# Optimization experiments

Measured on AMD Instinct MI355X. Metric: run time of the kernel, lower is better.

The kernel has to match this reference:

```python
import jax, jax.numpy as jnp
import numpy as np

V, C, D = 25, 64, 64          # joints, in_channels, out_channels
N, T = 64, 300                # batch, frames
WEIGHT = 2
GROUPS = [[0, 12], [13, 24]]
BN_EPS = 1e-5


def _inner_shift(A, graph_group, node, channels, weight):
    """Faithful numpy port of Modified_grouped_shift_gcn.inner_shift."""
    index_array = np.arange(node * channels).reshape(node, channels)
    copy = index_array.copy()
    for grp in graph_group:
        lb, ub = int(np.min(grp)), int(np.max(grp)) + 1
        for i in range(lb, ub):
            cur = A[i].copy()
            cur[i] = 0
            neighbors = np.nonzero(cur)[0]
            j = 0
            ci = i - lb + 1
            while j < channels:
                nxt = ci % (ub - lb) + lb
                if j < weight:
                    j += weight
                elif nxt == i:
                    j += weight
                    ci += 1
                elif nxt in neighbors:
                    index_array[i][j:j + weight] = copy[nxt][j:j + weight]
                    j += weight
                    ci += 1
                else:
                    index_array[i][j] = copy[nxt][j]
                    j += 1
                    ci += 1
    return index_array.flatten()


def _adjacency():
    # chain skeleton with self loops, binarized as in __init__
    A = np.zeros((V, V), dtype=np.float64)
    for i in range(V - 1):
        A[i, i + 1] = 1.0
        A[i + 1, i] = 1.0
    np.fill_diagonal(A, 1.0)
    return A


def setup_inputs() -> dict:
    key = jax.random.key(0)
    k0, k1, k2, k3 = jax.random.split(key, 4)
    A = _adjacency()
    shift_in = jnp.asarray(_inner_shift(A, GROUPS, V, C, WEIGHT), dtype=jnp.int32)
    shift_out = jnp.asarray(_inner_shift(A, GROUPS, V, D, WEIGHT), dtype=jnp.int32)
    x0 = jax.random.normal(k0, (N, C, T, V), dtype=jnp.float32)
    feature_mask = 0.1 * jax.random.normal(k1, (1, V, C), dtype=jnp.float32)
    W = jax.random.normal(k2, (C, D), dtype=jnp.float32) * np.float32(np.sqrt(1.0 / D))
    b = 0.01 * jax.random.normal(k3, (1, 1, D), dtype=jnp.float32)
    gamma = jnp.ones((V * D,), dtype=jnp.float32)
    beta = jnp.zeros((V * D,), dtype=jnp.float32)
    return {"x0": x0, "feature_mask": feature_mask, "W": W, "b": b,
            "gamma": gamma, "beta": beta,
            "shift_in": shift_in, "shift_out": shift_out}


def reference(x0, feature_mask, W, b, gamma, beta, shift_in, shift_out):
    n, c, t, v = x0.shape
    # (n, c, t, v) -> (n*t, v*c)
    x = jnp.transpose(x0, (0, 2, 3, 1)).reshape(n * t, v * c)
    # channel-wise shift gather (precomputed permutation)
    x = x[:, shift_in].reshape(n * t, v, c)
    # learned feature mask
    x = x * (jnp.tanh(feature_mask) + 1.0)
    # pointwise linear + bias
    x = jnp.einsum('nvc,cd->nvd', x, W) + b
    x = x.reshape(n * t, v * W.shape[1])
    # second shift gather
    x = x[:, shift_out]
    # BatchNorm1d, training mode (biased batch stats)
    mean = jnp.mean(x, axis=0)
    var = jnp.var(x, axis=0)
    x = (x - mean) * jax.lax.rsqrt(var + BN_EPS) * gamma + beta
    # back to (n, d, t, v), residual (in==out so down is identity), relu
    x = x.reshape(n, t, v, W.shape[1]).transpose(0, 3, 1, 2)
    return jax.nn.relu(x + x0)
```

## Files before the change

kernel.cpp:

```cpp
#include <hip/hip_runtime.h>
#include <math.h>

#define V_ 25
#define C_ 64
#define D_ 64
#define N_ 64
#define T_ 300
#define R_ (N_*T_)
#define K_ (V_*C_)
#define BN_EPS 1e-5f

#define WS_GM     0
#define WS_SCALE  1600
#define WS_SHIFT  3200
#define WS_VP     4800
#define WS_SUM    6400
#define WS_SQ     8000
#define WS_WBF    9600

#define P1_BLOCKS 1200

using bf16x8 = __attribute__((ext_vector_type(8))) short;
using f32x4  = __attribute__((ext_vector_type(4))) float;

__device__ __forceinline__ unsigned short f2bf(float f) {
    unsigned u = __float_as_uint(f);
    return (unsigned short)((u + 0x7FFFu + ((u >> 16) & 1u)) >> 16);
}

__global__ __launch_bounds__(256) void prep_tables(
    const float* __restrict__ fm, const float* __restrict__ W,
    const int* __restrict__ s_in, float* __restrict__ ws)
{
    int idx = blockIdx.x * 256 + threadIdx.x;
    if (idx < K_) {
        int jj  = s_in[idx];
        int off = (jj & 63) * 100 + (jj >> 6);
        unsigned mk = (unsigned)f2bf(tanhf(fm[idx]) + 1.0f);
        ((unsigned*)ws)[WS_GM + idx] = (mk << 16) | (unsigned)off;
    }
    if (idx < C_ * D_) ((unsigned short*)(ws + WS_WBF))[idx] = f2bf(W[idx]);
}

__global__ __launch_bounds__(256) void stats_reduce(
    const float* __restrict__ pbuf, float* __restrict__ ws)
{
    __shared__ float red[256];
    int jq = threadIdx.x & 15;
    int bq = threadIdx.x >> 4;
    int j  = blockIdx.x * 16 + jq;
    const float* p = pbuf + (size_t)(bq * 75) * 3200 + j;
    float s = 0.f;
    #pragma unroll 5
    for (int k = 0; k < 75; ++k)
        s += p[(size_t)k * 3200];
    red[threadIdx.x] = s;
    __syncthreads();
    if (bq < 8) red[threadIdx.x] += red[threadIdx.x + 128];
    __syncthreads();
    if (bq < 4) red[threadIdx.x] += red[threadIdx.x + 64];
    __syncthreads();
    if (bq < 2) red[threadIdx.x] += red[threadIdx.x + 32];
    __syncthreads();
    if (bq == 0) ws[WS_SUM + j] = red[jq] + red[jq + 16];
}

__global__ __launch_bounds__(256) void prep_scale_kernel(
    const float* __restrict__ gamma, const float* __restrict__ beta,
    const int* __restrict__ s_out, float* __restrict__ ws)
{
    int kk = blockIdx.x * 256 + threadIdx.x;
    if (kk < K_) {
        int dd = kk / 25;
        int v  = kk - dd * 25;
        int k  = v * 64 + dd;
        int jj = s_out[k];
        float mean = ws[WS_SUM + jj] * (1.0f / (float)R_);
        float var  = fmaf(-mean, mean, ws[WS_SQ + jj] * (1.0f / (float)R_));
        float inv  = rsqrtf(var + BN_EPS);
        float sc   = gamma[k] * inv;
        ws[WS_SCALE + kk] = sc;
        ws[WS_SHIFT + kk] = beta[k] - mean * sc;
        ((int*)ws)[WS_VP + kk] = jj;
    }
}

__device__ __forceinline__ void stage_xs(
    const float* __restrict__ xwin, float4* xs4, int tid)
{
    const float4* s4 = (const float4*)xwin;
    #pragma unroll
    for (int i = 0; i < 7; ++i) {
        int idx = i * 256 + tid;
        if (idx < 1600) {
            int c = idx / 25;
            int r = idx - c * 25;
            xs4[c * 25 + r] = s4[c * 1875 + r];
        }
    }
}

__device__ __forceinline__ void load_gmr(
    const unsigned* __restrict__ gmt, unsigned gmr[28], int lane, int w)
{
    int jw = lane & 3;
    int vh = lane >> 4;
    #pragma unroll
    for (int i = 0; i < 14; ++i) {
        int combo = i * 4 + w;
        int T  = combo >> 2;
        int q2 = combo & 3;
        int t  = T >> 1;
        int c0 = (T & 1) * 32 + q2 * 8 + jw * 2;
        int v  = t * 4 + vh;
        int kb = (v < V_) ? (v * 64 + c0) : c0;
        gmr[2 * i]     = gmt[kb];
        gmr[2 * i + 1] = gmt[kb + 1];
    }
}

__device__ __forceinline__ void build_afm(
    const float* xs, unsigned* a_fm32, const unsigned gmr[28], int lane, int w)
{
    int m  = lane >> 2;
    int jw = lane & 3;
    int dt = m & 3;
    #pragma unroll
    for (int i = 0; i < 14; ++i) {
        int combo = i * 4 + w;
        int T  = combo >> 2;
        int q2 = combo & 3;
        unsigned g0 = gmr[2 * i], g1 = gmr[2 * i + 1];
        float m0 = __uint_as_float(g0 & 0xFFFF0000u);
        float m1 = __uint_as_float(g1 & 0xFFFF0000u);
        float f0 = xs[(g0 & 0xFFFFu) + dt * 25] * m0;
        float f1 = xs[(g1 & 0xFFFFu) + dt * 25] * m1;
        a_fm32[(T * 64 + q2 * 16 + m) * 4 + jw] =
            (unsigned)f2bf(f0) | ((unsigned)f2bf(f1) << 16);
    }
}

__global__ __launch_bounds__(256, 4) void pass1_stats(
    const float* __restrict__ x0, const float* __restrict__ bg,
    const float* __restrict__ ws, float* __restrict__ pbuf)
{
    __shared__ __align__(16) float4 xs4[1600];
    __shared__ __align__(16) unsigned a_fm32[3584];
    const float* xs = (const float*)xs4;
    const bf16x8* afp = (const bf16x8*)a_fm32;

    int tid = threadIdx.x;
    int lane = tid & 63, w = tid >> 6;
    int l15 = lane & 15, q = lane >> 4;
    int d = w * 16 + l15;

    const unsigned short* Wbf = (const unsigned short*)(ws + WS_WBF);
    bf16x8 bfrag0, bfrag1;
    #pragma unroll
    for (int j = 0; j < 8; ++j) {
        bfrag0[j] = (short)Wbf[(q * 8 + j) * 64 + d];
        bfrag1[j] = (short)Wbf[(32 + q * 8 + j) * 64 + d];
    }
    float breg = bg[d];

    unsigned gmr[28];
    load_gmr((const unsigned*)ws + WS_GM, gmr, lane, w);

    float sums[7], sqs[7];
    #pragma unroll
    for (int t = 0; t < 7; ++t) { sums[t] = 0.f; sqs[t] = 0.f; }

    #pragma unroll 1
    for (int st = 0; st < 4; ++st) {
        int r0 = blockIdx.x * 16 + st * 4;
        int n  = r0 / 300;
        int t0 = r0 - n * 300;
        const float* xwin = x0 + (size_t)n * 480000 + t0 * 25;

        stage_xs(xwin, xs4, tid);
        __syncthreads();
        build_afm(xs, a_fm32, gmr, lane, w);
        __syncthreads();

        #pragma unroll
        for (int t = 0; t < 7; ++t) {
            bf16x8 a0 = afp[(t * 2 + 0) * 64 + lane];
            bf16x8 a1 = afp[(t * 2 + 1) * 64 + lane];
            f32x4 acc = {0.f, 0.f, 0.f, 0.f};
            acc = __builtin_amdgcn_mfma_f32_16x16x32_bf16(a0, bfrag0, acc, 0, 0, 0);
            acc = __builtin_amdgcn_mfma_f32_16x16x32_bf16(a1, bfrag1, acc, 0, 0, 0);
            #pragma unroll
            for (int r = 0; r < 4; ++r) {
                float y = acc[r] + breg;
                sums[t] += y;
                sqs[t]   = fmaf(y, y, sqs[t]);
            }
        }
        __syncthreads();
    }

    float* pout = pbuf + (size_t)blockIdx.x * 3200;
    #pragma unroll
    for (int t = 0; t < 7; ++t) {
        int v = t * 4 + q;
        if (v < V_) {
            __builtin_nontemporal_store(sums[t], &pout[v * 64 + d]);
            __builtin_nontemporal_store(sqs[t],  &pout[1600 + v * 64 + d]);
        }
    }
}

__global__ __launch_bounds__(256, 4) void pass2_out(
    const float* __restrict__ x0, const float* __restrict__ bg,
    const float* __restrict__ ws, float* __restrict__ out)
{
    __shared__ __align__(16) char smem[25600 + 14336];
    float4* xs4   = (float4*)smem;
    const float* xs = (const float*)smem;
    float* y_lds  = (float*)smem;
    unsigned* a_fm32 = (unsigned*)(smem + 25600);
    const bf16x8* afp = (const bf16x8*)a_fm32;

    int tid = threadIdx.x;
    int lane = tid & 63, w = tid >> 6;
    int l15 = lane & 15, q = lane >> 4;
    int d = w * 16 + l15;

    const unsigned short* Wbf = (const unsigned short*)(ws + WS_WBF);
    bf16x8 bfrag0, bfrag1;
    #pragma unroll
    for (int j = 0; j < 8; ++j) {
        bfrag0[j] = (short)Wbf[(q * 8 + j) * 64 + d];
        bfrag1[j] = (short)Wbf[(32 + q * 8 + j) * 64 + d];
    }
    float breg = bg[d];

    unsigned gmr[28];
    load_gmr((const unsigned*)ws + WS_GM, gmr, lane, w);

    int r0 = blockIdx.x * 4;
    int n  = r0 / 300;
    int t0 = r0 - n * 300;
    const float* xwin = x0 + (size_t)n * 480000 + t0 * 25;

    stage_xs(xwin, xs4, tid);
    __syncthreads();
    build_afm(xs, a_fm32, gmr, lane, w);
    __syncthreads();

    #pragma unroll
    for (int t = 0; t < 7; ++t) {
        bf16x8 a0 = afp[(t * 2 + 0) * 64 + lane];
        bf16x8 a1 = afp[(t * 2 + 1) * 64 + lane];
        f32x4 acc = {0.f, 0.f, 0.f, 0.f};
        acc = __builtin_amdgcn_mfma_f32_16x16x32_bf16(a0, bfrag0, acc, 0, 0, 0);
        acc = __builtin_amdgcn_mfma_f32_16x16x32_bf16(a1, bfrag1, acc, 0, 0, 0);
        int v = t * 4 + q;
        if (v < V_) {
            #pragma unroll
            for (int r = 0; r < 4; ++r)
                y_lds[d * 100 + r * 25 + v] = acc[r] + breg;
        }
    }
    __syncthreads();

    const float* scp = ws + WS_SCALE;
    const float* shp = ws + WS_SHIFT;
    const int*   vpp = (const int*)ws + WS_VP;
    #pragma unroll
    for (int i = 0; i < 25; ++i) {
        int e   = i * 256 + tid;
        int dd  = e / 100;
        int rem = e - dd * 100;
        int dt  = rem / 25;
        int v   = rem - dt * 25;
        int kk  = dd * 25 + v;
        int jj  = vpp[kk];
        float z = y_lds[(jj & 63) * 100 + dt * 25 + (jj >> 6)];
        int ga  = (n * 64 + dd) * 7500 + (t0 + dt) * 25 + v;
        float val = fmaf(z, scp[kk], shp[kk]) + x0[ga];
        __builtin_nontemporal_store(fmaxf(val, 0.f), &out[ga]);
    }
}

extern "C" void kernel_launch(void* const* d_in, const int* in_sizes, int n_in,
                              void* d_out, int out_size, void* d_ws, size_t ws_size,
                              hipStream_t stream)
{
    const float* x0    = (const float*)d_in[0];
    const float* fm    = (const float*)d_in[1];
    const float* W     = (const float*)d_in[2];
    const float* b     = (const float*)d_in[3];
    const float* gamma = (const float*)d_in[4];
    const float* beta  = (const float*)d_in[5];
    const int*   s_in  = (const int*)d_in[6];
    const int*   s_out = (const int*)d_in[7];
    float* out = (float*)d_out;
    float* ws  = (float*)d_ws;

    prep_tables<<<16, 256, 0, stream>>>(fm, W, s_in, ws);
    pass1_stats<<<P1_BLOCKS, 256, 0, stream>>>(x0, b, ws, out);
    stats_reduce<<<200, 256, 0, stream>>>(out, ws);
    prep_scale_kernel<<<7, 256, 0, stream>>>(gamma, beta, s_out, ws);
    pass2_out<<<R_ / 4, 256, 0, stream>>>(x0, b, ws, out);
}
```

Measured before the change: 309.7 us.

## Double-buffer pass1 with async global-to-LDS loads and vectorize pass2 epilogue

Pass1 becomes a persistent grid of 512 blocks that stride over windows. It double-buffers the x0 tile in LDS using global_load_lds, so the next window's load overlaps with building and multiplying the current one. Pass2 reuses the staged x0 tile from LDS as the residual instead of reloading it from global memory, and uses precomputed per-element scale, shift and index tables so the epilogue can do float4 loads and stores. The gains are traded for larger workspace tables, more LDS, and a different occupancy hint.

```diff
diff --git a/kernel.cpp b/kernel.cpp
--- a/kernel.cpp
+++ b/kernel.cpp
@@ -10,22 +10,37 @@
 #define K_ (V_*C_)
 #define BN_EPS 1e-5f
 
-#define WS_GM     0
-#define WS_SCALE  1600
-#define WS_SHIFT  3200
-#define WS_VP     4800
-#define WS_SUM    6400
-#define WS_SQ     8000
-#define WS_WBF    9600
-
-#define P1_BLOCKS 1200
+#define WS_GM    0
+#define WS_SUM   1600
+#define WS_SQ    3200
+#define WS_WBF   4800
+#define WS_SC2   6848
+#define WS_SH2   13248
+#define WS_YO    19648
+
+#define P1_GRID  512
+#define NWIN     4800
 
 using bf16x8 = __attribute__((ext_vector_type(8))) short;
 using f32x4  = __attribute__((ext_vector_type(4))) float;
+using i32x4  = __attribute__((ext_vector_type(4))) int;
 
 __device__ __forceinline__ unsigned short f2bf(float f) {
     unsigned u = __float_as_uint(f);
     return (unsigned short)((u + 0x7FFFu + ((u >> 16) & 1u)) >> 16);
+}
+
+__device__ __forceinline__ void gload16(const void* g, void* l) {
+    __builtin_amdgcn_global_load_lds(
+        (const __attribute__((address_space(1))) void*)g,
+        (__attribute__((address_space(3))) void*)l, 16, 0, 0);
+}
+
+__device__ __forceinline__ void barrier_lds() {
+    asm volatile("s_waitcnt lgkmcnt(0)" ::: "memory");
+    __builtin_amdgcn_sched_barrier(0);
+    __builtin_amdgcn_s_barrier();
+    __builtin_amdgcn_sched_barrier(0);
 }
 
 __global__ __launch_bounds__(256) void prep_tables(
@@ -49,10 +64,10 @@
     int jq = threadIdx.x & 15;
     int bq = threadIdx.x >> 4;
     int j  = blockIdx.x * 16 + jq;
-    const float* p = pbuf + (size_t)(bq * 75) * 3200 + j;
+    const float* p = pbuf + (size_t)(bq * 32) * 3200 + j;
     float s = 0.f;
-    #pragma unroll 5
-    for (int k = 0; k < 75; ++k)
+    #pragma unroll 8
+    for (int k = 0; k < 32; ++k)
         s += p[(size_t)k * 3200];
     red[threadIdx.x] = s;
     __syncthreads();
@@ -69,34 +84,40 @@
     const float* __restrict__ gamma, const float* __restrict__ beta,
     const int* __restrict__ s_out, float* __restrict__ ws)
 {
-    int kk = blockIdx.x * 256 + threadIdx.x;
-    if (kk < K_) {
-        int dd = kk / 25;
-        int v  = kk - dd * 25;
-        int k  = v * 64 + dd;
-        int jj = s_out[k];
+    int e = blockIdx.x * 256 + threadIdx.x;
+    if (e < 6400) {
+        int dd  = e / 100;
+        int rem = e - dd * 100;
+        int dt  = rem / 25;
+        int v   = rem - dt * 25;
+        int k   = v * 64 + dd;
+        int jj  = s_out[k];
         float mean = ws[WS_SUM + jj] * (1.0f / (float)R_);
         float var  = fmaf(-mean, mean, ws[WS_SQ + jj] * (1.0f / (float)R_));
         float inv  = rsqrtf(var + BN_EPS);
         float sc   = gamma[k] * inv;
-        ws[WS_SCALE + kk] = sc;
-        ws[WS_SHIFT + kk] = beta[k] - mean * sc;
-        ((int*)ws)[WS_VP + kk] = jj;
-    }
-}
-
-__device__ __forceinline__ void stage_xs(
-    const float* __restrict__ xwin, float4* xs4, int tid)
+        ws[WS_SC2 + e] = sc;
+        ws[WS_SH2 + e] = beta[k] - mean * sc;
+        ((unsigned*)ws)[WS_YO + e] = (unsigned)((jj & 63) * 100 + dt * 25 + (jj >> 6));
+    }
+}
+
+__device__ __forceinline__ const float* win_ptr(const float* x0, int wi) {
+    int r0 = wi * 4;
+    int n  = r0 / 300;
+    int t0 = r0 - n * 300;
+    return x0 + (size_t)n * 480000 + t0 * 25;
+}
+
+__device__ __forceinline__ void issue_stage(
+    const float* __restrict__ xwin, float4* dst, const int gOff[7], int tid)
 {
     const float4* s4 = (const float4*)xwin;
     #pragma unroll
     for (int i = 0; i < 7; ++i) {
         int idx = i * 256 + tid;
-        if (idx < 1600) {
-            int c = idx / 25;
-            int r = idx - c * 25;
-            xs4[c * 25 + r] = s4[c * 1875 + r];
-        }
+        if (idx < 1600)
+            gload16(s4 + gOff[i], dst + idx);
     }
 }
 
@@ -140,13 +161,12 @@
     }
 }
 
-__global__ __launch_bounds__(256, 4) void pass1_stats(
+__global__ __launch_bounds__(256) void pass1_stats(
     const float* __restrict__ x0, const float* __restrict__ bg,
     const float* __restrict__ ws, float* __restrict__ pbuf)
 {
-    __shared__ __align__(16) float4 xs4[1600];
+    __shared__ __align__(16) float4 xs2[2][1600];
     __shared__ __align__(16) unsigned a_fm32[3584];
-    const float* xs = (const float*)xs4;
     const bf16x8* afp = (const bf16x8*)a_fm32;
 
     int tid = threadIdx.x;
@@ -166,21 +186,31 @@
     unsigned gmr[28];
     load_gmr((const unsigned*)ws + WS_GM, gmr, lane, w);
 
+    int gOff[7];
+    #pragma unroll
+    for (int i = 0; i < 7; ++i) {
+        int idx = i * 256 + tid;
+        int c = idx / 25;
+        int r = idx - c * 25;
+        gOff[i] = c * 1875 + r;
+    }
+
     float sums[7], sqs[7];
     #pragma unroll
     for (int t = 0; t < 7; ++t) { sums[t] = 0.f; sqs[t] = 0.f; }
 
-    #pragma unroll 1
-    for (int st = 0; st < 4; ++st) {
-        int r0 = blockIdx.x * 16 + st * 4;
-        int n  = r0 / 300;
-        int t0 = r0 - n * 300;
-        const float* xwin = x0 + (size_t)n * 480000 + t0 * 25;
-
-        stage_xs(xwin, xs4, tid);
+    int wi = blockIdx.x;
+    issue_stage(win_ptr(x0, wi), xs2[0], gOff, tid);
+    int cur = 0;
+
+    while (true) {
         __syncthreads();
-        build_afm(xs, a_fm32, gmr, lane, w);
-        __syncthreads();
+        int nwi = wi + P1_GRID;
+        if (nwi < NWIN)
+            issue_stage(win_ptr(x0, nwi), xs2[cur ^ 1], gOff, tid);
+
+        build_afm((const float*)xs2[cur], a_fm32, gmr, lane, w);
+        barrier_lds();
 
         #pragma unroll
         for (int t = 0; t < 7; ++t) {
@@ -196,7 +226,8 @@
                 sqs[t]   = fmaf(y, y, sqs[t]);
             }
         }
-        __syncthreads();
+        if (nwi >= NWIN) break;
+        wi = nwi; cur ^= 1;
     }
 
     float* pout = pbuf + (size_t)blockIdx.x * 3200;
@@ -210,22 +241,36 @@
     }
 }
 
-__global__ __launch_bounds__(256, 4) void pass2_out(
+__global__ __launch_bounds__(256, 3) void pass2_out(
     const float* __restrict__ x0, const float* __restrict__ bg,
     const float* __restrict__ ws, float* __restrict__ out)
 {
-    __shared__ __align__(16) char smem[25600 + 14336];
-    float4* xs4   = (float4*)smem;
-    const float* xs = (const float*)smem;
-    float* y_lds  = (float*)smem;
-    unsigned* a_fm32 = (unsigned*)(smem + 25600);
-    const bf16x8* afp = (const bf16x8*)a_fm32;
+    __shared__ __align__(16) float4 xs4[1600];
+    __shared__ __align__(16) float  yu[6400];
+    const float* xs = (const float*)xs4;
+    unsigned* a_fm32 = (unsigned*)yu;
+    const bf16x8* afp = (const bf16x8*)yu;
+    float* y_lds = yu;
 
     int tid = threadIdx.x;
     int lane = tid & 63, w = tid >> 6;
     int l15 = lane & 15, q = lane >> 4;
     int d = w * 16 + l15;
 
+    int r0 = blockIdx.x * 4;
+    int n  = r0 / 300;
+    int t0 = r0 - n * 300;
+
+    int gOff[7];
+    #pragma unroll
+    for (int i = 0; i < 7; ++i) {
+        int idx = i * 256 + tid;
+        int c = idx / 25;
+        int r = idx - c * 25;
+        gOff[i] = c * 1875 + r;
+    }
+    issue_stage(x0 + (size_t)n * 480000 + t0 * 25, xs4, gOff, tid);
+
     const unsigned short* Wbf = (const unsigned short*)(ws + WS_WBF);
     bf16x8 bfrag0, bfrag1;
     #pragma unroll
@@ -234,27 +279,24 @@
         bfrag1[j] = (short)Wbf[(32 + q * 8 + j) * 64 + d];
     }
     float breg = bg[d];
-
     unsigned gmr[28];
     load_gmr((const unsigned*)ws + WS_GM, gmr, lane, w);
 
-    int r0 = blockIdx.x * 4;
-    int n  = r0 / 300;
-    int t0 = r0 - n * 300;
-    const float* xwin = x0 + (size_t)n * 480000 + t0 * 25;
-
-    stage_xs(xwin, xs4, tid);
     __syncthreads();
     build_afm(xs, a_fm32, gmr, lane, w);
     __syncthreads();
 
+    bf16x8 af[14];
+    #pragma unroll
+    for (int t2 = 0; t2 < 14; ++t2)
+        af[t2] = afp[t2 * 64 + lane];
+    __syncthreads();
+
     #pragma unroll
     for (int t = 0; t < 7; ++t) {
-        bf16x8 a0 = afp[(t * 2 + 0) * 64 + lane];
-        bf16x8 a1 = afp[(t * 2 + 1) * 64 + lane];
         f32x4 acc = {0.f, 0.f, 0.f, 0.f};
-        acc = __builtin_amdgcn_mfma_f32_16x16x32_bf16(a0, bfrag0, acc, 0, 0, 0);
-        acc = __builtin_amdgcn_mfma_f32_16x16x32_bf16(a1, bfrag1, acc, 0, 0, 0);
+        acc = __builtin_amdgcn_mfma_f32_16x16x32_bf16(af[2 * t],     bfrag0, acc, 0, 0, 0);
+        acc = __builtin_amdgcn_mfma_f32_16x16x32_bf16(af[2 * t + 1], bfrag1, acc, 0, 0, 0);
         int v = t * 4 + q;
         if (v < V_) {
             #pragma unroll
@@ -264,22 +306,28 @@
     }
     __syncthreads();
 
-    const float* scp = ws + WS_SCALE;
-    const float* shp = ws + WS_SHIFT;
-    const int*   vpp = (const int*)ws + WS_VP;
-    #pragma unroll
-    for (int i = 0; i < 25; ++i) {
-        int e   = i * 256 + tid;
-        int dd  = e / 100;
-        int rem = e - dd * 100;
-        int dt  = rem / 25;
-        int v   = rem - dt * 25;
-        int kk  = dd * 25 + v;
-        int jj  = vpp[kk];
-        float z = y_lds[(jj & 63) * 100 + dt * 25 + (jj >> 6)];
-        int ga  = (n * 64 + dd) * 7500 + (t0 + dt) * 25 + v;
-        float val = fmaf(z, scp[kk], shp[kk]) + x0[ga];
-        __builtin_nontemporal_store(fmaxf(val, 0.f), &out[ga]);
+    const f32x4* sc4 = (const f32x4*)(ws + WS_SC2);
+    const f32x4* sh4 = (const f32x4*)(ws + WS_SH2);
+    const i32x4* yo4 = (const i32x4*)((const int*)ws + WS_YO);
+    const f32x4* rs4 = (const f32x4*)xs;
+    float* outbase = out + (size_t)n * 480000 + t0 * 25;
+    #pragma unroll
+    for (int i = 0; i < 7; ++i) {
+        int idx = i * 256 + tid;
+        if (idx < 1600) {
+            int dd  = idx / 25;
+            int pos = idx - dd * 25;
+            f32x4 sc = sc4[idx];
+            f32x4 sh = sh4[idx];
+            i32x4 yo = yo4[idx];
+            f32x4 rs = rs4[idx];
+            f32x4 o;
+            o[0] = fmaxf(fmaf(y_lds[yo[0]], sc[0], sh[0]) + rs[0], 0.f);
+            o[1] = fmaxf(fmaf(y_lds[yo[1]], sc[1], sh[1]) + rs[1], 0.f);
+            o[2] = fmaxf(fmaf(y_lds[yo[2]], sc[2], sh[2]) + rs[2], 0.f);
+            o[3] = fmaxf(fmaf(y_lds[yo[3]], sc[3], sh[3]) + rs[3], 0.f);
+            __builtin_nontemporal_store(o, (f32x4*)(outbase + dd * 7500) + pos);
+        }
     }
 }
 
@@ -299,8 +347,8 @@
     float* ws  = (float*)d_ws;
 
     prep_tables<<<16, 256, 0, stream>>>(fm, W, s_in, ws);
-    pass1_stats<<<P1_BLOCKS, 256, 0, stream>>>(x0, b, ws, out);
+    pass1_stats<<<P1_GRID, 256, 0, stream>>>(x0, b, ws, out);
     stats_reduce<<<200, 256, 0, stream>>>(out, ws);
-    prep_scale_kernel<<<7, 256, 0, stream>>>(gamma, beta, s_out, ws);
-    pass2_out<<<R_ / 4, 256, 0, stream>>>(x0, b, ws, out);
-}
+    prep_scale_kernel<<<25, 256, 0, stream>>>(gamma, beta, s_out, ws);
+    pass2_out<<<NWIN, 256, 0, stream>>>(x0, b, ws, out);
+}
```

Result: faster. 273.0 us (-11.8%).
